# Kernel optimization log

Measured on AMD Instinct MI355X. Metric: run time of the kernel, lower is better.

## Reference

```python
import jax, jax.numpy as jnp
import numpy as np

N_WIN = 7      # region grid (BiFormer default)
NUM_HEADS = 8
TOPK = 4
EPS = 1e-5

def layernorm(x, g, b):
    mu = x.mean(-1, keepdims=True)
    var = ((x - mu) ** 2).mean(-1, keepdims=True)
    return (x - mu) * jax.lax.rsqrt(var + EPS) * g + b

def bilevel_routing_attn(x, wqkv, bqkv, wo, bo):
    B, H, W, C = x.shape
    h, w = H // N_WIN, W // N_WIN          # region size (8,8)
    R, r = N_WIN * N_WIN, h * w            # 49 regions, 64 tokens each
    d = C // NUM_HEADS
    scale = 1.0 / jnp.sqrt(jnp.asarray(d, x.dtype))
    qkv = x @ wqkv + bqkv                  # (B,H,W,3C)
    q, k, v = jnp.split(qkv, 3, axis=-1)
    def to_regions(t):
        t = t.reshape(B, N_WIN, h, N_WIN, w, C).transpose(0, 1, 3, 2, 4, 5)
        return t.reshape(B, R, r, C)
    qr, kr, vr = to_regions(q), to_regions(k), to_regions(v)
    # coarse region-level routing
    q_reg = qr.mean(2)                     # (B,R,C)
    k_reg = kr.mean(2)
    logits = jnp.einsum('brc,bsc->brs', q_reg, k_reg)   # (B,R,R)
    _, idx = jax.lax.top_k(logits, TOPK)   # (B,R,TOPK)
    # gather top-k regions' k/v: out[b,i,j] = kr[b, idx[b,i,j]]
    idx_e = idx[:, :, :, None, None]       # (B,R,TOPK,1,1)
    kg = jnp.take_along_axis(kr[:, None], idx_e, axis=2).reshape(B, R, TOPK * r, C)
    vg = jnp.take_along_axis(vr[:, None], idx_e, axis=2).reshape(B, R, TOPK * r, C)
    # fine-grained multi-head attention within routed regions
    qh = qr.reshape(B, R, r, NUM_HEADS, d)
    kh = kg.reshape(B, R, TOPK * r, NUM_HEADS, d)
    vh = vg.reshape(B, R, TOPK * r, NUM_HEADS, d)
    scores = jnp.einsum('brqhd,brkhd->brhqk', qh, kh) * scale
    attn = jax.nn.softmax(scores, axis=-1)
    out = jnp.einsum('brhqk,brkhd->brqhd', attn, vh).reshape(B, R, r, C)
    # regions back to image layout
    out = out.reshape(B, N_WIN, N_WIN, h, w, C).transpose(0, 1, 3, 2, 4, 5)
    out = out.reshape(B, H, W, C)
    return out @ wo + bo

def mlp(x, w1, bm1, w2, bm2):
    return jax.nn.gelu(x @ w1 + bm1) @ w2 + bm2

def setup_inputs() -> dict:
    key = jax.random.key(0)
    ks = jax.random.split(key, 5)
    C = 256
    s = lambda fan: 1.0 / np.sqrt(fan)
    return {
        'x': jax.random.normal(ks[0], (8, 56, 56, C), jnp.float32),
        'ln1_g': jnp.ones((C,), jnp.float32),
        'ln1_b': jnp.zeros((C,), jnp.float32),
        'wqkv': jax.random.normal(ks[1], (C, 3 * C), jnp.float32) * s(C),
        'bqkv': jnp.zeros((3 * C,), jnp.float32),
        'wo': jax.random.normal(ks[2], (C, C), jnp.float32) * s(C),
        'bo': jnp.zeros((C,), jnp.float32),
        'ln2_g': jnp.ones((C,), jnp.float32),
        'ln2_b': jnp.zeros((C,), jnp.float32),
        'w1': jax.random.normal(ks[3], (C, 4 * C), jnp.float32) * s(C),
        'bm1': jnp.zeros((4 * C,), jnp.float32),
        'w2': jax.random.normal(ks[4], (4 * C, C), jnp.float32) * s(4 * C),
        'bm2': jnp.zeros((C,), jnp.float32),
    }

def reference(x, ln1_g, ln1_b, wqkv, bqkv, wo, bo, ln2_g, ln2_b, w1, bm1, w2, bm2):
    x = x + bilevel_routing_attn(layernorm(x, ln1_g, ln1_b), wqkv, bqkv, wo, bo)
    x = x + mlp(layernorm(x, ln2_g, ln2_b), w1, bm1, w2, bm2)
    return x
```

## Files before the change

### kernel.cpp

```cpp
#include <hip/hip_runtime.h>
#include <math.h>

#define CDIM 256
#define QKVDIM 768
#define NHEADS 8
#define DHEAD 32
#define NWIN 7
#define NREG 49
#define TK 4
static constexpr int NROWS = 8 * 56 * 56;

typedef __attribute__((ext_vector_type(8))) short s16x8;
typedef __attribute__((ext_vector_type(4))) float f32x4;
typedef __attribute__((ext_vector_type(16))) float f32x16;
typedef unsigned short ushort_t;

union U4 { unsigned u[4]; s16x8 v; };

__device__ __forceinline__ ushort_t bfr(float f) {
    unsigned u = __float_as_uint(f);
    unsigned r = (u + 0x7FFFu + ((u >> 16) & 1u)) >> 16;
    return (ushort_t)r;
}
__device__ __forceinline__ float gelu_f(float x) {
    float u = 0.7978845608028654f * (x + 0.044715f * x * x * x);
    float e = __expf(2.0f * u);
    float t = 1.0f - __fdividef(2.0f, e + 1.0f);
    return 0.5f * x * (1.0f + t);
}
__device__ __forceinline__ void glds16(const void* g, void* l) {
    __builtin_amdgcn_global_load_lds((const __attribute__((address_space(1))) void*)g,
                                     (__attribute__((address_space(3))) void*)l, 16, 0, 0);
}
template <int N>
__device__ __forceinline__ void waitvm() {
    if constexpr (N == 0) asm volatile("s_waitcnt vmcnt(0)" ::: "memory");
    else if constexpr (N == 3) asm volatile("s_waitcnt vmcnt(3)" ::: "memory");
    else if constexpr (N == 4) asm volatile("s_waitcnt vmcnt(4)" ::: "memory");
    else if constexpr (N == 6) asm volatile("s_waitcnt vmcnt(6)" ::: "memory");
    else if constexpr (N == 8) asm volatile("s_waitcnt vmcnt(8)" ::: "memory");
}
__device__ __forceinline__ void barrier_raw() {
    asm volatile("s_barrier" ::: "memory");
}
__device__ __forceinline__ f32x16 zero16() {
    f32x16 z;
#pragma unroll
    for (int i = 0; i < 16; i++) z[i] = 0.f;
    return z;
}

__global__ __launch_bounds__(256) void ln_kernel(const float* __restrict__ x,
                                                 const float* __restrict__ g,
                                                 const float* __restrict__ bparam,
                                                 ushort_t* __restrict__ y) {
    int wave = threadIdx.x >> 6, lane = threadIdx.x & 63;
    int row = blockIdx.x * 4 + wave;
    const float4* xr = (const float4*)(x + (size_t)row * CDIM);
    float4 v = xr[lane];
    float s = v.x + v.y + v.z + v.w;
    float s2 = v.x * v.x + v.y * v.y + v.z * v.z + v.w * v.w;
#pragma unroll
    for (int off = 32; off; off >>= 1) {
        s += __shfl_xor(s, off, 64);
        s2 += __shfl_xor(s2, off, 64);
    }
    float mu = s * (1.0f / CDIM);
    float rstd = rsqrtf(s2 * (1.0f / CDIM) - mu * mu + 1e-5f);
    float4 gv = ((const float4*)g)[lane];
    float4 bv = ((const float4*)bparam)[lane];
    ushort4 o;
    o.x = bfr((v.x - mu) * rstd * gv.x + bv.x);
    o.y = bfr((v.y - mu) * rstd * gv.y + bv.y);
    o.z = bfr((v.z - mu) * rstd * gv.z + bv.z);
    o.w = bfr((v.w - mu) * rstd * gv.w + bv.w);
    *(ushort4*)(y + (size_t)row * CDIM + lane * 4) = o;
}

__global__ __launch_bounds__(256) void ymean_kernel(const float* __restrict__ x,
                                                    const float* __restrict__ g,
                                                    const float* __restrict__ bparam,
                                                    float* __restrict__ ymean) {
    int blk = blockIdx.x;
    int b = blk / NREG, rid = blk % NREG;
    int ai = rid / NWIN, aj = rid % NWIN;
    int w = threadIdx.x >> 6, lane = threadIdx.x & 63;
    float4 gv = ((const float4*)g)[lane];
    float4 bv = ((const float4*)bparam)[lane];
    float4 acc = {0.f, 0.f, 0.f, 0.f};
    for (int it = 0; it < 16; it++) {
        int t = it * 4 + w;
        size_t row = ((size_t)(b * 56 + ai * 8 + (t >> 3))) * 56 + aj * 8 + (t & 7);
        float4 v = ((const float4*)(x + row * CDIM))[lane];
        float s = v.x + v.y + v.z + v.w;
        float s2 = v.x * v.x + v.y * v.y + v.z * v.z + v.w * v.w;
#pragma unroll
        for (int off = 32; off; off >>= 1) {
            s += __shfl_xor(s, off, 64);
            s2 += __shfl_xor(s2, off, 64);
        }
        float mu = s * (1.0f / CDIM);
        float rstd = rsqrtf(s2 * (1.0f / CDIM) - mu * mu + 1e-5f);
        acc.x += (v.x - mu) * rstd * gv.x + bv.x;
        acc.y += (v.y - mu) * rstd * gv.y + bv.y;
        acc.z += (v.z - mu) * rstd * gv.z + bv.z;
        acc.w += (v.w - mu) * rstd * gv.w + bv.w;
    }
    __shared__ float red[4][CDIM];
    *(float4*)&red[w][lane * 4] = acc;
    __syncthreads();
    if (w == 0) {
        float4 r0 = *(float4*)&red[0][lane * 4];
        float4 r1 = *(float4*)&red[1][lane * 4];
        float4 r2 = *(float4*)&red[2][lane * 4];
        float4 r3 = *(float4*)&red[3][lane * 4];
        float4 o;
        o.x = (r0.x + r1.x + r2.x + r3.x) * (1.0f / 64.0f);
        o.y = (r0.y + r1.y + r2.y + r3.y) * (1.0f / 64.0f);
        o.z = (r0.z + r1.z + r2.z + r3.z) * (1.0f / 64.0f);
        o.w = (r0.w + r1.w + r2.w + r3.w) * (1.0f / 64.0f);
        *(float4*)(ymean + (size_t)blk * CDIM + lane * 4) = o;
    }
}

__global__ __launch_bounds__(256) void regproj_kernel(const float* __restrict__ ymean,
                                                      const float* __restrict__ wqkv,
                                                      const float* __restrict__ bqkv,
                                                      float* __restrict__ qreg,
                                                      float* __restrict__ kreg) {
    int blk = blockIdx.x;
    __shared__ float ym[CDIM];
    ym[threadIdx.x] = ymean[(size_t)blk * CDIM + threadIdx.x];
    __syncthreads();
    int c = threadIdx.x;
    float sq = 0.f, sk = 0.f;
    for (int k = 0; k < CDIM; k++) {
        float yv = ym[k];
        sq = fmaf(yv, wqkv[(size_t)k * QKVDIM + c], sq);
        sk = fmaf(yv, wqkv[(size_t)k * QKVDIM + CDIM + c], sk);
    }
    qreg[(size_t)blk * CDIM + c] = sq + bqkv[c];
    kreg[(size_t)blk * CDIM + c] = sk + bqkv[CDIM + c];
}

__global__ __launch_bounds__(256) void wtrans_kernel(const float* __restrict__ src,
                                                     ushort_t* __restrict__ dst,
                                                     int K, int N) {
    __shared__ float t[32][33];
    int tx = threadIdx.x & 31, ty = threadIdx.x >> 5;
    int n0 = blockIdx.x * 32, k0 = blockIdx.y * 32;
#pragma unroll
    for (int i = 0; i < 4; i++) t[ty + i * 8][tx] = src[(size_t)(k0 + ty + i * 8) * N + n0 + tx];
    __syncthreads();
#pragma unroll
    for (int i = 0; i < 4; i++)
        dst[(size_t)(n0 + ty + i * 8) * K + k0 + tx] = bfr(t[tx][ty + i * 8]);
}

__global__ __launch_bounds__(256) void vtrans_kernel(const ushort_t* __restrict__ qkvbf,
                                                     ushort_t* __restrict__ vt) {
    __shared__ ushort_t t[32][34];
    int tx = threadIdx.x & 31, ty = threadIdx.x >> 5;
    int t0 = blockIdx.x * 32, c0 = blockIdx.y * 32, b = blockIdx.z;
#pragma unroll
    for (int i = 0; i < 4; i++)
        t[ty + i * 8][tx] = qkvbf[((size_t)b * 3136 + t0 + ty + i * 8) * QKVDIM + 512 + c0 + tx];
    __syncthreads();
#pragma unroll
    for (int i = 0; i < 4; i++)
        vt[((size_t)b * CDIM + c0 + ty + i * 8) * 3136 + t0 + tx] = t[tx][ty + i * 8];
}

template <int BM, int BN, int MODE>
__global__ __launch_bounds__(256) void mgemm(const ushort_t* __restrict__ A,
                                             const ushort_t* __restrict__ WT,
                                             const float* __restrict__ bias,
                                             const float* __restrict__ res,
                                             float* __restrict__ outf,
                                             ushort_t* __restrict__ outb,
                                             int N, int K) {
    constexpr int WM = BM / 2, WN = BN / 2, MI = WM / 16, NI = WN / 16;
    constexpr int RA = BM / 64, RB = BN / 64, L = RA + RB;
    constexpr int BUFB = (BM + BN) * 64;
    __shared__ __align__(16) char smem[3 * BUFB];
    ushort_t* Cs = (ushort_t*)smem;
    const int tid = threadIdx.x, lane = tid & 63, w = tid >> 6;
    const int wm = w >> 1, wn = w & 1;

    const int gx = gridDim.x;
    const int nwg = gx * gridDim.y;
    const int bid = blockIdx.y * gx + blockIdx.x;
    const int lbid = (bid & 7) * (nwg >> 3) + (bid >> 3);
    const int tm = (lbid / gx) * BM, tn = (lbid % gx) * BN;

    f32x4 acc[MI][NI];
#pragma unroll
    for (int i = 0; i < MI; i++)
#pragma unroll
        for (int j = 0; j < NI; j++) acc[i][j] = (f32x4){0.f, 0.f, 0.f, 0.f};

    size_t aoff[RA], boff[RB];
    int adst[RA], bdst[RB];
#pragma unroll
    for (int p = 0; p < RA; p++) {
        int row = (p * 4 + w) * 16 + (lane >> 2);
        int slot = lane & 3;
        int mr = (row >> 1) & 3;
        aoff[p] = (size_t)(tm + row) * K + ((slot ^ mr) * 8);
        adst[p] = (p * 4 + w) * 1024;
    }
#pragma unroll
    for (int p = 0; p < RB; p++) {
        int row = (p * 4 + w) * 16 + (lane >> 2);
        int slot = lane & 3;
        int mr = (row >> 1) & 3;
        boff[p] = (size_t)(tn + row) * K + ((slot ^ mr) * 8);
        bdst[p] = BM * 64 + (p * 4 + w) * 1024;
    }
    const int fr = lane & 15, sl = lane >> 4;
    int roa[MI], rob[NI];
#pragma unroll
    for (int i = 0; i < MI; i++) {
        int rowa = wm * WM + i * 16 + fr;
        roa[i] = rowa * 64 + ((sl ^ ((rowa >> 1) & 3)) * 16);
    }
#pragma unroll
    for (int j = 0; j < NI; j++) {
        int rowb = wn * WN + j * 16 + fr;
        rob[j] = BM * 64 + rowb * 64 + ((sl ^ ((rowb >> 1) & 3)) * 16);
    }

    auto stage = [&](int buf, int k0) {
        char* base = smem + buf * BUFB;
#pragma unroll
        for (int p = 0; p < RA; p++) glds16(A + aoff[p] + k0, base + adst[p]);
#pragma unroll
        for (int p = 0; p < RB; p++) glds16(WT + boff[p] + k0, base + bdst[p]);
    };

    const int NT = K >> 5;
    stage(0, 0);
    stage(1, 32);
    int cb = 0, sb = 2;
    for (int kt = 0; kt < NT; ++kt) {
        if (kt + 2 < NT) {
            stage(sb, (kt + 2) * 32);
            sb = (sb + 1 < 3) ? sb + 1 : 0;
            waitvm<2 * L>();
        } else if (kt + 1 < NT) {
            waitvm<L>();
        } else {
            waitvm<0>();
        }
        barrier_raw();
        const char* base = smem + cb * BUFB;
        s16x8 af[MI], bfv[NI];
#pragma unroll
        for (int i = 0; i < MI; i++) af[i] = *(const s16x8*)(base + roa[i]);
#pragma unroll
        for (int j = 0; j < NI; j++) bfv[j] = *(const s16x8*)(base + rob[j]);
#pragma unroll
        for (int i = 0; i < MI; i++)
#pragma unroll
            for (int j = 0; j < NI; j++)
                acc[i][j] = __builtin_amdgcn_mfma_f32_16x16x32_bf16(af[i], bfv[j], acc[i][j], 0, 0, 0);
        barrier_raw();
        cb = (cb + 1 < 3) ? cb + 1 : 0;
    }

    const int cl = lane & 15, gq = lane >> 4;
    if constexpr (MODE == 0 || MODE == 2) {
#pragma unroll
        for (int hh = 0; hh < 2; hh++) {
            if (wm == hh) {
#pragma unroll
                for (int j = 0; j < NI; j++) {
                    int lcol = wn * WN + j * 16 + cl;
                    int col = tn + lcol;
                    float bb = bias[col];
#pragma unroll
                    for (int i = 0; i < MI; i++) {
#pragma unroll
                        for (int r = 0; r < 4; r++) {
                            float v = acc[i][j][r] + bb;
                            ushort_t ov;
                            if (MODE == 0)
                                ov = bfr(col < 256 ? v * 0.17677669529663687f : v);
                            else
                                ov = bfr(gelu_f(v));
                            Cs[(i * 16 + gq * 4 + r) * 136 + lcol] = ov;
                        }
                    }
                }
            }
            __syncthreads();
            {
                int row_l = tid >> 2;
                int cbx = (tid & 3) * 8;
                ushort_t* gbase = outb + (size_t)(tm + hh * 64 + row_l) * N + tn;
#pragma unroll
                for (int c = 0; c < 4; c++) {
                    int col = cbx + c * 32;
                    *(s16x8*)(gbase + col) = *(const s16x8*)&Cs[row_l * 136 + col];
                }
            }
            if (hh == 0) __syncthreads();
        }
    } else {
#pragma unroll
        for (int j = 0; j < NI; j++) {
            int col = tn + wn * WN + j * 16 + cl;
            float bb = bias[col];
#pragma unroll
            for (int i = 0; i < MI; i++) {
                int rowb = tm + wm * WM + i * 16 + gq * 4;
#pragma unroll
                for (int r = 0; r < 4; r++) {
                    float v = acc[i][j][r] + bb;
                    size_t off = (size_t)(rowb + r) * N + col;
                    outf[off] = v + res[off];
                }
            }
        }
    }
}

__global__ __launch_bounds__(64) void routing_kernel(const float* __restrict__ qreg,
                                                     const float* __restrict__ kreg,
                                                     int* __restrict__ idx) {
    int b = blockIdx.x / NREG;
    int row = blockIdx.x % NREG;
    int lane = threadIdx.x;
    float myv = -INFINITY;
    if (lane < NREG) {
        const float* qv = qreg + ((size_t)b * NREG + row) * CDIM;
        const float* kv = kreg + ((size_t)b * NREG + lane) * CDIM;
        float s = 0.f;
        for (int c = 0; c < CDIM; c++) s += qv[c] * kv[c];
        myv = s;
    }
    for (int t = 0; t < TK; t++) {
        float v = myv;
        int ix = lane;
#pragma unroll
        for (int off = 32; off; off >>= 1) {
            float ov = __shfl_xor(v, off, 64);
            int oi = __shfl_xor(ix, off, 64);
            if (ov > v || (ov == v && oi < ix)) { v = ov; ix = oi; }
        }
        if (lane == 0) idx[((size_t)b * NREG + row) * TK + t] = ix;
        if (lane == ix) myv = -INFINITY;
    }
}

__global__ __launch_bounds__(256) void attn2_kernel(const ushort_t* __restrict__ qk,
                                                    const ushort_t* __restrict__ vt,
                                                    const int* __restrict__ idx,
                                                    ushort_t* __restrict__ outb) {
    int wid = blockIdx.x * 4 + (threadIdx.x >> 6);
    int lane = threadIdx.x & 63;
    int g = lane >> 5, col = lane & 31;
    int qh = wid & 1;
    int h = (wid >> 1) & 7;
    int rr = wid >> 4;
    int rid = rr % NREG, b = rr / NREG;
    int ai = rid / NWIN, aj = rid % NWIN;

    int qtok = qh * 32 + col;
    size_t qrow_g = ((size_t)(b * 56 + ai * 8 + (qtok >> 3))) * 56 + aj * 8 + (qtok & 7);
    const s16x8 bq0 = *(const s16x8*)(qk + qrow_g * QKVDIM + h * 32 + g * 8);
    const s16x8 bq1 = *(const s16x8*)(qk + qrow_g * QKVDIM + h * 32 + 16 + g * 8);

    const int* ip = idx + (size_t)rr * TK;
    int regs[4] = {ip[0], ip[1], ip[2], ip[3]};

    float m_run = -1e30f, l_run = 0.f;
    f32x16 o = zero16();
    const size_t vtrowbase = ((size_t)(b * CDIM + h * 32 + col)) * 3136;

#pragma unroll
    for (int rc = 0; rc < 4; rc++) {
        int reg = regs[rc];
        int rai = reg / NWIN, raj = reg % NWIN;
        s16x8 ka[2][2];
#pragma unroll
        for (int mf = 0; mf < 2; mf++) {
            int ktok = mf * 32 + col;
            size_t krow_g = ((size_t)(b * 56 + rai * 8 + (ktok >> 3))) * 56 + raj * 8 + (ktok & 7);
#pragma unroll
            for (int kd = 0; kd < 2; kd++)
                ka[mf][kd] = *(const s16x8*)(qk + krow_g * QKVDIM + 256 + h * 32 + kd * 16 + g * 8);
        }
        f32x16 s0 = zero16(), s1 = zero16();
        s0 = __builtin_amdgcn_mfma_f32_32x32x16_bf16(ka[0][0], bq0, s0, 0, 0, 0);
        s0 = __builtin_amdgcn_mfma_f32_32x32x16_bf16(ka[0][1], bq1, s0, 0, 0, 0);
        s1 = __builtin_amdgcn_mfma_f32_32x32x16_bf16(ka[1][0], bq0, s1, 0, 0, 0);
        s1 = __builtin_amdgcn_mfma_f32_32x32x16_bf16(ka[1][1], bq1, s1, 0, 0, 0);

        float tmax = -1e30f;
#pragma unroll
        for (int i = 0; i < 16; i++) tmax = fmaxf(tmax, fmaxf(s0[i], s1[i]));
        tmax = fmaxf(tmax, __shfl_xor(tmax, 32, 64));

        float m_new = fmaxf(m_run, tmax);
        float f = __expf(m_run - m_new);
        l_run *= f;
#pragma unroll
        for (int r = 0; r < 16; r++) {
            int orow = (r & 3) + 8 * (r >> 2) + 4 * g;
            float fr2 = __shfl(f, orow, 64);
            o[r] *= fr2;
        }
        m_run = m_new;

        float tsum = 0.f;
#pragma unroll
        for (int i = 0; i < 16; i++) {
            s0[i] = __expf(s0[i] - m_run);
            s1[i] = __expf(s1[i] - m_run);
            tsum += s0[i] + s1[i];
        }
        l_run += tsum + __shfl_xor(tsum, 32, 64);

#define PVSTEP(SS, CC, KS)                                                              \
    {                                                                                   \
        unsigned wa = (unsigned)bfr(SS[CC * 8 + 0]) | ((unsigned)bfr(SS[CC * 8 + 1]) << 16); \
        unsigned wb_ = (unsigned)bfr(SS[CC * 8 + 2]) | ((unsigned)bfr(SS[CC * 8 + 3]) << 16); \
        unsigned wc = (unsigned)bfr(SS[CC * 8 + 4]) | ((unsigned)bfr(SS[CC * 8 + 5]) << 16); \
        unsigned wd = (unsigned)bfr(SS[CC * 8 + 6]) | ((unsigned)bfr(SS[CC * 8 + 7]) << 16); \
        unsigned sxa = (unsigned)__shfl_xor((int)wa, 32, 64);                           \
        unsigned sxb = (unsigned)__shfl_xor((int)wb_, 32, 64);                          \
        unsigned sxc = (unsigned)__shfl_xor((int)wc, 32, 64);                           \
        unsigned sxd = (unsigned)__shfl_xor((int)wd, 32, 64);                           \
        U4 pw;                                                                          \
        pw.u[0] = g ? sxc : wa;                                                         \
        pw.u[1] = g ? sxd : wb_;                                                        \
        pw.u[2] = g ? wc : sxa;                                                         \
        pw.u[3] = g ? wd : sxb;                                                         \
        const s16x8 vb = *(const s16x8*)(vt + vtrowbase + (size_t)(rai * 8 + KS * 2 + g) * 56 + raj * 8); \
        o = __builtin_amdgcn_mfma_f32_32x32x16_bf16(pw.v, vb, o, 0, 0, 0);              \
    }
        PVSTEP(s0, 0, 0)
        PVSTEP(s0, 1, 1)
        PVSTEP(s1, 0, 2)
        PVSTEP(s1, 1, 3)
#undef PVSTEP
    }

#pragma unroll
    for (int r = 0; r < 16; r++) {
        int orow = (r & 3) + 8 * (r >> 2) + 4 * g;
        float lr = __shfl(l_run, orow, 64);
        float val = o[r] / lr;
        int tok = qh * 32 + orow;
        size_t row_g = ((size_t)(b * 56 + ai * 8 + (tok >> 3))) * 56 + aj * 8 + (tok & 7);
        outb[row_g * 256 + h * 32 + col] = bfr(val);
    }
}

extern "C" void kernel_launch(void* const* d_in, const int* in_sizes, int n_in,
                              void* d_out, int out_size, void* d_ws, size_t ws_size,
                              hipStream_t stream) {
    const float* x    = (const float*)d_in[0];
    const float* ln1g = (const float*)d_in[1];
    const float* ln1b = (const float*)d_in[2];
    const float* wqkv = (const float*)d_in[3];
    const float* bqkv = (const float*)d_in[4];
    const float* wo   = (const float*)d_in[5];
    const float* bo   = (const float*)d_in[6];
    const float* ln2g = (const float*)d_in[7];
    const float* ln2b = (const float*)d_in[8];
    const float* w1   = (const float*)d_in[9];
    const float* bm1  = (const float*)d_in[10];
    const float* w2   = (const float*)d_in[11];
    const float* bm2  = (const float*)d_in[12];
    float* out = (float*)d_out;
    char* ws = (char*)d_ws;

    ushort_t* ws_qkvbf = (ushort_t*)(ws);
    ushort_t* ws_hbf   = (ushort_t*)(ws + 38535168);
    ushort_t* ws_ybf   = (ushort_t*)(ws + 89915392);
    ushort_t* ws_vt    = (ushort_t*)(ws + 102760448);
    ushort_t* ws_attn  = (ushort_t*)(ws + 115605504);
    float*    ws_ymean = (float*)(ws + 128450560);
    float*    ws_qreg  = (float*)(ws + 128851968);
    float*    ws_kreg  = (float*)(ws + 129253376);
    int*      ws_idx   = (int*)(ws + 129654784);
    ushort_t* ws_wqkvT = (ushort_t*)(ws + 129661056);
    ushort_t* ws_woT   = (ushort_t*)(ws + 130054272);
    ushort_t* ws_w1T   = (ushort_t*)(ws + 130185344);
    ushort_t* ws_w2T   = (ushort_t*)(ws + 130709632);

    const int M = NROWS;

    wtrans_kernel<<<dim3(768 / 32, 256 / 32), 256, 0, stream>>>(wqkv, ws_wqkvT, 256, 768);
    wtrans_kernel<<<dim3(256 / 32, 256 / 32), 256, 0, stream>>>(wo, ws_woT, 256, 256);
    wtrans_kernel<<<dim3(1024 / 32, 256 / 32), 256, 0, stream>>>(w1, ws_w1T, 256, 1024);
    wtrans_kernel<<<dim3(256 / 32, 1024 / 32), 256, 0, stream>>>(w2, ws_w2T, 1024, 256);
    ln_kernel<<<M / 4, 256, 0, stream>>>(x, ln1g, ln1b, ws_ybf);
    ymean_kernel<<<8 * NREG, 256, 0, stream>>>(x, ln1g, ln1b, ws_ymean);
    regproj_kernel<<<8 * NREG, 256, 0, stream>>>(ws_ymean, wqkv, bqkv, ws_qreg, ws_kreg);
    routing_kernel<<<8 * NREG, 64, 0, stream>>>(ws_qreg, ws_kreg, ws_idx);
    mgemm<128, 128, 0><<<dim3(QKVDIM / 128, M / 128), 256, 0, stream>>>(
        ws_ybf, ws_wqkvT, bqkv, nullptr, nullptr, ws_qkvbf, QKVDIM, CDIM);
    vtrans_kernel<<<dim3(3136 / 32, 256 / 32, 8), 256, 0, stream>>>(ws_qkvbf, ws_vt);
    attn2_kernel<<<8 * NREG * NHEADS * 2 / 4, 256, 0, stream>>>(ws_qkvbf, ws_vt, ws_idx, ws_attn);
    mgemm<128, 64, 1><<<dim3(CDIM / 64, M / 128), 256, 0, stream>>>(
        ws_attn, ws_woT, bo, x, out, nullptr, CDIM, CDIM);
    ln_kernel<<<M / 4, 256, 0, stream>>>(out, ln2g, ln2b, ws_ybf);
    mgemm<128, 128, 2><<<dim3(1024 / 128, M / 128), 256, 0, stream>>>(
        ws_ybf, ws_w1T, bm1, nullptr, nullptr, ws_hbf, 1024, CDIM);
    mgemm<128, 64, 3><<<dim3(CDIM / 64, M / 128), 256, 0, stream>>>(
        ws_hbf, ws_w2T, bm2, out, out, nullptr, CDIM, 1024);
}
```

Before: 315.9 us.

## Load GEMM B fragments directly from global and double-buffer A with K=64 tiles

The GEMM kernel no longer stages the weight (B) tile through LDS. Each wave loads its B fragments straight from global memory into registers, while only the A tile is staged via global_load_lds. The K step grows from 32 to 64 and the pipeline drops from a triple buffer to a double buffer, with an 8-slot XOR swizzle for A. This is meant to cut LDS traffic and barriers per K, at the cost of redundant global/L2 reads of B across waves and a shallower prefetch. The new layout also hard-codes 4 A-stage loads per thread, which assumes BM=128.

```diff
diff --git a/kernel.cpp b/kernel.cpp
--- a/kernel.cpp
+++ b/kernel.cpp
@@ -35,10 +35,8 @@
 template <int N>
 __device__ __forceinline__ void waitvm() {
     if constexpr (N == 0) asm volatile("s_waitcnt vmcnt(0)" ::: "memory");
-    else if constexpr (N == 3) asm volatile("s_waitcnt vmcnt(3)" ::: "memory");
+    else if constexpr (N == 2) asm volatile("s_waitcnt vmcnt(2)" ::: "memory");
     else if constexpr (N == 4) asm volatile("s_waitcnt vmcnt(4)" ::: "memory");
-    else if constexpr (N == 6) asm volatile("s_waitcnt vmcnt(6)" ::: "memory");
-    else if constexpr (N == 8) asm volatile("s_waitcnt vmcnt(8)" ::: "memory");
 }
 __device__ __forceinline__ void barrier_raw() {
     asm volatile("s_barrier" ::: "memory");
@@ -180,9 +178,7 @@
                                              ushort_t* __restrict__ outb,
                                              int N, int K) {
     constexpr int WM = BM / 2, WN = BN / 2, MI = WM / 16, NI = WN / 16;
-    constexpr int RA = BM / 64, RB = BN / 64, L = RA + RB;
-    constexpr int BUFB = (BM + BN) * 64;
-    __shared__ __align__(16) char smem[3 * BUFB];
+    __shared__ __align__(16) char smem[2 * BM * 128];
     ushort_t* Cs = (ushort_t*)smem;
     const int tid = threadIdx.x, lane = tid & 63, w = tid >> 6;
     const int wm = w >> 1, wn = w & 1;
@@ -199,73 +195,68 @@
 #pragma unroll
         for (int j = 0; j < NI; j++) acc[i][j] = (f32x4){0.f, 0.f, 0.f, 0.f};
 
-    size_t aoff[RA], boff[RB];
-    int adst[RA], bdst[RB];
-#pragma unroll
-    for (int p = 0; p < RA; p++) {
-        int row = (p * 4 + w) * 16 + (lane >> 2);
-        int slot = lane & 3;
-        int mr = (row >> 1) & 3;
-        aoff[p] = (size_t)(tm + row) * K + ((slot ^ mr) * 8);
+    size_t aoff[4];
+    int adst[4];
+#pragma unroll
+    for (int p = 0; p < 4; p++) {
+        int row = (p * 4 + w) * 8 + (lane >> 3);
+        int slot = lane & 7;
+        aoff[p] = (size_t)(tm + row) * K + ((slot ^ (row & 7)) * 8);
         adst[p] = (p * 4 + w) * 1024;
     }
-#pragma unroll
-    for (int p = 0; p < RB; p++) {
-        int row = (p * 4 + w) * 16 + (lane >> 2);
-        int slot = lane & 3;
-        int mr = (row >> 1) & 3;
-        boff[p] = (size_t)(tn + row) * K + ((slot ^ mr) * 8);
-        bdst[p] = BM * 64 + (p * 4 + w) * 1024;
-    }
     const int fr = lane & 15, sl = lane >> 4;
-    int roa[MI], rob[NI];
+    int rbase[MI], r7[MI];
 #pragma unroll
     for (int i = 0; i < MI; i++) {
         int rowa = wm * WM + i * 16 + fr;
-        roa[i] = rowa * 64 + ((sl ^ ((rowa >> 1) & 3)) * 16);
-    }
-#pragma unroll
-    for (int j = 0; j < NI; j++) {
-        int rowb = wn * WN + j * 16 + fr;
-        rob[j] = BM * 64 + rowb * 64 + ((sl ^ ((rowb >> 1) & 3)) * 16);
-    }
+        rbase[i] = rowa * 128;
+        r7[i] = rowa & 7;
+    }
+    const ushort_t* bp[NI];
+#pragma unroll
+    for (int j = 0; j < NI; j++)
+        bp[j] = WT + (size_t)(tn + wn * WN + j * 16 + fr) * K + sl * 8;
 
     auto stage = [&](int buf, int k0) {
-        char* base = smem + buf * BUFB;
-#pragma unroll
-        for (int p = 0; p < RA; p++) glds16(A + aoff[p] + k0, base + adst[p]);
-#pragma unroll
-        for (int p = 0; p < RB; p++) glds16(WT + boff[p] + k0, base + bdst[p]);
+        char* base = smem + buf * BM * 128;
+#pragma unroll
+        for (int p = 0; p < 4; p++) glds16(A + aoff[p] + k0, base + adst[p]);
     };
 
-    const int NT = K >> 5;
+    const int NT = K >> 6;
     stage(0, 0);
-    stage(1, 32);
-    int cb = 0, sb = 2;
+    int buf = 0;
     for (int kt = 0; kt < NT; ++kt) {
-        if (kt + 2 < NT) {
-            stage(sb, (kt + 2) * 32);
-            sb = (sb + 1 < 3) ? sb + 1 : 0;
-            waitvm<2 * L>();
-        } else if (kt + 1 < NT) {
-            waitvm<L>();
-        } else {
-            waitvm<0>();
-        }
+        const int k0 = kt * 64;
+        s16x8 b0[NI];
+#pragma unroll
+        for (int j = 0; j < NI; j++) b0[j] = *(const s16x8*)(bp[j] + k0);
+        waitvm<NI>();
         barrier_raw();
-        const char* base = smem + cb * BUFB;
-        s16x8 af[MI], bfv[NI];
-#pragma unroll
-        for (int i = 0; i < MI; i++) af[i] = *(const s16x8*)(base + roa[i]);
-#pragma unroll
-        for (int j = 0; j < NI; j++) bfv[j] = *(const s16x8*)(base + rob[j]);
+        s16x8 b1[NI];
+#pragma unroll
+        for (int j = 0; j < NI; j++) b1[j] = *(const s16x8*)(bp[j] + k0 + 32);
+        if (kt + 1 < NT) stage(buf ^ 1, k0 + 64);
+        const char* base = smem + buf * BM * 128;
+        s16x8 af[MI];
 #pragma unroll
         for (int i = 0; i < MI; i++)
+            af[i] = *(const s16x8*)(base + rbase[i] + ((sl ^ r7[i]) * 16));
+#pragma unroll
+        for (int i = 0; i < MI; i++)
 #pragma unroll
             for (int j = 0; j < NI; j++)
-                acc[i][j] = __builtin_amdgcn_mfma_f32_16x16x32_bf16(af[i], bfv[j], acc[i][j], 0, 0, 0);
+                acc[i][j] = __builtin_amdgcn_mfma_f32_16x16x32_bf16(af[i], b0[j], acc[i][j], 0, 0, 0);
+#pragma unroll
+        for (int i = 0; i < MI; i++)
+            af[i] = *(const s16x8*)(base + rbase[i] + (((4 + sl) ^ r7[i]) * 16));
+#pragma unroll
+        for (int i = 0; i < MI; i++)
+#pragma unroll
+            for (int j = 0; j < NI; j++)
+                acc[i][j] = __builtin_amdgcn_mfma_f32_16x16x32_bf16(af[i], b1[j], acc[i][j], 0, 0, 0);
         barrier_raw();
-        cb = (cb + 1 < 3) ? cb + 1 : 0;
+        buf ^= 1;
     }
 
     const int cl = lane & 15, gq = lane >> 4;
```

New measurement: 349.7 us. 1.11x slower.
